# Kernel tuning notes

Measured on AMD Instinct MI355X. Metric: run time of the kernel, lower is better.

## Reference

```python
import jax, jax.numpy as jnp
import numpy as np
import math

LEVEL_SHAPES = [(100, 152), (50, 76), (25, 38), (13, 19)]
BS, E, NH, NL, NP = 2, 256, 8, 4, 4


def _grid_init_bias(num_heads, num_levels, num_points):
    # faithful to MultiScaleDeformableAttention.init_weights sampling_offsets bias
    thetas = jnp.arange(num_heads, dtype=jnp.float32) * (2.0 * math.pi / num_heads)
    grid = jnp.stack([jnp.cos(thetas), jnp.sin(thetas)], -1)  # [H,2]
    grid = grid / jnp.max(jnp.abs(grid), axis=-1, keepdims=True)
    grid = jnp.tile(grid[:, None, None, :], (1, num_levels, num_points, 1))  # [H,L,P,2]
    scale = jnp.arange(1, num_points + 1, dtype=jnp.float32)[None, None, :, None]
    return (grid * scale).reshape(-1)


def setup_inputs() -> dict:
    key = jax.random.key(0)
    ks = jax.random.split(key, 10)
    nv = sum(h * w for h, w in LEVEL_SHAPES)  # 20197
    nq = nv
    query = jax.random.normal(ks[0], (BS, nq, E), dtype=jnp.float32)
    value = jax.random.normal(ks[1], (BS, nv, E), dtype=jnp.float32)
    reference_points = jax.random.uniform(ks[2], (BS, nq, NL, 2), dtype=jnp.float32)
    spatial_shapes = jnp.array(LEVEL_SHAPES, dtype=jnp.int32)
    sizes = [h * w for h, w in LEVEL_SHAPES]
    level_start_index = jnp.array(np.cumsum([0] + sizes)[:-1], dtype=jnp.int32)
    s = 1.0 / math.sqrt(E)
    # Linear params stored as [in, out]; y = x @ W + b
    Wv = jax.random.normal(ks[3], (E, E), dtype=jnp.float32) * s
    bv = jnp.zeros((E,), jnp.float32)
    Wso = jax.random.normal(ks[4], (E, NH * NL * NP * 2), dtype=jnp.float32) * 0.01
    bso = _grid_init_bias(NH, NL, NP)
    Waw = jax.random.normal(ks[5], (E, NH * NL * NP), dtype=jnp.float32) * 0.01
    baw = jnp.zeros((NH * NL * NP,), jnp.float32)
    Wo = jax.random.normal(ks[6], (E, E), dtype=jnp.float32) * s
    bo = jnp.zeros((E,), jnp.float32)
    return dict(query=query, value=value, reference_points=reference_points,
                spatial_shapes=spatial_shapes, level_start_index=level_start_index,
                Wv=Wv, bv=bv, Wso=Wso, bso=bso, Waw=Waw, baw=baw, Wo=Wo, bo=bo)


def _bilinear_sample(vl, loc, h, w):
    # vl: [bs, nh, h*w, d]; loc: [bs, nq, nh, P, 2] normalized in [0,1]
    # matches F.grid_sample(mode='bilinear', padding_mode='zeros', align_corners=False)
    bs, nh, _, d = vl.shape
    nq, P = loc.shape[1], loc.shape[3]
    x = loc[..., 0] * w - 0.5
    y = loc[..., 1] * h - 0.5
    x0 = jnp.floor(x).astype(jnp.int32); x1 = x0 + 1
    y0 = jnp.floor(y).astype(jnp.int32); y1 = y0 + 1
    wx1 = x - x0; wx0 = 1.0 - wx1
    wy1 = y - y0; wy0 = 1.0 - wy1

    def gather(ix, iy):
        valid = ((ix >= 0) & (ix < w) & (iy >= 0) & (iy < h)).astype(vl.dtype)
        idx = jnp.clip(iy, 0, h - 1) * w + jnp.clip(ix, 0, w - 1)  # [bs,nq,nh,P]
        idx = jnp.transpose(idx, (0, 2, 1, 3)).reshape(bs, nh, nq * P)
        g = jnp.take_along_axis(vl, idx[..., None], axis=2)  # [bs,nh,nq*P,d]
        g = g.reshape(bs, nh, nq, P, d).transpose(0, 2, 1, 3, 4)  # [bs,nq,nh,P,d]
        return g * valid[..., None]

    return (gather(x0, y0) * (wx0 * wy0)[..., None]
            + gather(x1, y0) * (wx1 * wy0)[..., None]
            + gather(x0, y1) * (wx0 * wy1)[..., None]
            + gather(x1, y1) * (wx1 * wy1)[..., None])


def reference(query, value, reference_points, spatial_shapes, level_start_index,
              Wv, bv, Wso, bso, Waw, baw, Wo, bo):
    bs, nq, e = query.shape
    nv = value.shape[1]
    nh, nl, npt = NH, NL, NP
    d = e // nh
    shapes = np.asarray(spatial_shapes)          # static level shapes
    starts = np.asarray(level_start_index)

    v = (value @ Wv + bv).reshape(bs, nv, nh, d).transpose(0, 2, 1, 3)  # [bs,nh,nv,d]
    so = (query @ Wso + bso).reshape(bs, nq, nh, nl, npt, 2)
    aw = jax.nn.softmax((query @ Waw + baw).reshape(bs, nq, nh, nl * npt), axis=-1)
    aw = aw.reshape(bs, nq, nh, nl, npt)

    # offset normalizer is (w, h) per level
    offset_norm = jnp.stack([spatial_shapes[:, 1], spatial_shapes[:, 0]], -1).astype(query.dtype)
    loc = reference_points[:, :, None, :, None, :] + so / offset_norm[None, None, None, :, None, :]

    out = jnp.zeros((bs, nq, nh, d), dtype=query.dtype)
    for l in range(nl):
        h, w = int(shapes[l, 0]), int(shapes[l, 1])
        s = int(starts[l])
        vl = v[:, :, s:s + h * w, :]                      # [bs,nh,h*w,d]
        sampled = _bilinear_sample(vl, loc[:, :, :, l], h, w)  # [bs,nq,nh,P,d]
        out = out + jnp.einsum('bqhpd,bqhp->bqhd', sampled, aw[:, :, :, l])

    out = out.reshape(bs, nq, e) @ Wo + bo
    return out + query  # identity residual (dropout in eval mode)
```

## Files before the change

### kernel.cpp

```cpp
#include <hip/hip_runtime.h>
#include <hip/hip_bf16.h>
#include <math.h>

constexpr int kBS = 2;
constexpr int kNQ = 20197;
constexpr int kNV = 20197;
constexpr int kNH = 8;
constexpr int kM  = kBS * kNQ;
constexpr int kMpad = 40448;

__constant__ int cLH[4] = {100, 50, 25, 13};
__constant__ int cLW[4] = {152, 76, 38, 19};
__constant__ int cLS[4] = {0, 15200, 19000, 19950};

typedef __bf16 bf16x8 __attribute__((ext_vector_type(8)));
typedef float  f32x4  __attribute__((ext_vector_type(4)));

__device__ __forceinline__ unsigned short f2bf(float x) {
    unsigned u = __float_as_uint(x);
    return (unsigned short)((u + 0x7fffu + ((u >> 16) & 1u)) >> 16);
}
__device__ __forceinline__ unsigned pack2(float a, float b) {
    return (unsigned)f2bf(a) | ((unsigned)f2bf(b) << 16);
}
__device__ __forceinline__ void gload_lds16(const void* g, void* s) {
    __builtin_amdgcn_global_load_lds(
        (const __attribute__((address_space(1))) void*)g,
        (__attribute__((address_space(3))) void*)s, 16, 0, 0);
}

__global__ __launch_bounds__(256) void prep_wt(
    const float* __restrict__ src, unsigned short* __restrict__ dst,
    int total, int N)
{
    int i = blockIdx.x * 256 + threadIdx.x;
    if (i >= total) return;
    int n = i >> 8, k = i & 255;
    dst[i] = f2bf(src[k * N + n]);
}

template<bool ABF16, bool OUTBF16, bool RES>
__global__ __launch_bounds__(256) void gemm_mfma(
    const void* __restrict__ Av, const __hip_bfloat16* __restrict__ BT,
    const float* __restrict__ bias, const float* __restrict__ res,
    void* __restrict__ Cv, int M, int N)
{
    constexpr int APITCH = ABF16 ? 32 : 40;
    __shared__ __hip_bfloat16 As[128 * APITCH];
    __shared__ __hip_bfloat16 Bs[128 * 32];

    const int t = threadIdx.x;
    const int wave = t >> 6, lane = t & 63;
    const int quad = lane >> 4, l16 = lane & 15;
    const int mw = (wave & 1) * 64, nw = (wave >> 1) * 64;
    const int m0 = blockIdx.y * 128, n0 = blockIdx.x * 128;
    const int sm = t >> 1;
    const int sh = (t & 1) * 16;

    f32x4 acc[4][4] = {};

    for (int k0 = 0; k0 < 256; k0 += 32) {
        __syncthreads();
        {
            const char* bt = (const char*)BT;
            #pragma unroll
            for (int j = 0; j < 2; ++j) {
                int off = j * 4096 + t * 16;
                int row = off >> 6, kb = off & 63;
                gload_lds16(bt + (size_t)(n0 + row) * 512 + k0 * 2 + kb,
                            (char*)Bs + off);
            }
        }
        if constexpr (ABF16) {
            const char* ab = (const char*)Av;
            #pragma unroll
            for (int j = 0; j < 2; ++j) {
                int off = j * 4096 + t * 16;
                int row = off >> 6, kb = off & 63;
                gload_lds16(ab + (size_t)(m0 + row) * 512 + k0 * 2 + kb,
                            (char*)As + off);
            }
        } else {
            const float* af = (const float*)Av;
            float4 f0 = make_float4(0.f, 0.f, 0.f, 0.f), f1 = f0, f2 = f0, f3 = f0;
            if (m0 + sm < M) {
                const float4* p = (const float4*)(af + (size_t)(m0 + sm) * 256 + k0 + sh);
                f0 = p[0]; f1 = p[1]; f2 = p[2]; f3 = p[3];
            }
            uint4 q0 = make_uint4(pack2(f0.x, f0.y), pack2(f0.z, f0.w),
                                  pack2(f1.x, f1.y), pack2(f1.z, f1.w));
            uint4 q1 = make_uint4(pack2(f2.x, f2.y), pack2(f2.z, f2.w),
                                  pack2(f3.x, f3.y), pack2(f3.z, f3.w));
            uint4* dst = (uint4*)(void*)&As[sm * APITCH + sh];
            dst[0] = q0; dst[1] = q1;
        }
        __syncthreads();
        bf16x8 afr[4], bfr[4];
        #pragma unroll
        for (int mt = 0; mt < 4; ++mt)
            afr[mt] = *(const bf16x8*)(const void*)&As[(mw + mt * 16 + l16) * APITCH + quad * 8];
        #pragma unroll
        for (int nt = 0; nt < 4; ++nt)
            bfr[nt] = *(const bf16x8*)(const void*)&Bs[(nw + nt * 16 + l16) * 32 + quad * 8];
        #pragma unroll
        for (int mt = 0; mt < 4; ++mt)
            #pragma unroll
            for (int nt = 0; nt < 4; ++nt)
                acc[mt][nt] = __builtin_amdgcn_mfma_f32_16x16x32_bf16(
                    afr[mt], bfr[nt], acc[mt][nt], 0, 0, 0);
    }

    #pragma unroll
    for (int nt = 0; nt < 4; ++nt) {
        int col = n0 + nw + nt * 16 + l16;
        float bvv = bias[col];
        #pragma unroll
        for (int mt = 0; mt < 4; ++mt) {
            #pragma unroll
            for (int i = 0; i < 4; ++i) {
                int row = m0 + mw + mt * 16 + quad * 4 + i;
                if (row < M) {
                    float val = acc[mt][nt][i] + bvv;
                    if constexpr (RES) val += res[(size_t)row * N + col];
                    if constexpr (OUTBF16)
                        ((unsigned short*)Cv)[(size_t)row * N + col] = f2bf(val);
                    else
                        ((float*)Cv)[(size_t)row * N + col] = val;
                }
            }
        }
    }
}

__global__ __launch_bounds__(128) void msda_sample(
    const __hip_bfloat16* __restrict__ v,
    const float* __restrict__ so,
    const float* __restrict__ logits,
    const float* __restrict__ rp,
    __hip_bfloat16* __restrict__ mid)
{
    const int bq = blockIdx.x;
    const int b  = bq >= kNQ;
    const int t  = threadIdx.x;

    __shared__ int   sOff[128 * 5];
    __shared__ float sW[128 * 5];

    {
        const int h = t >> 4, l = (t >> 2) & 3;
        float2 sv = *(const float2*)(so + (size_t)bq * 256 + 2 * t);
        float  aa = logits[(size_t)bq * 128 + t];
        float2 rr = *(const float2*)(rp + (size_t)bq * 8 + l * 2);
        float mx = aa;
        #pragma unroll
        for (int s = 8; s >= 1; s >>= 1) mx = fmaxf(mx, __shfl_xor(mx, s, 16));
        float e = __expf(aa - mx);
        float sum = e;
        #pragma unroll
        for (int s = 8; s >= 1; s >>= 1) sum += __shfl_xor(sum, s, 16);
        float w = e / sum;

        const int ww = cLW[l], hh = cLH[l];
        const float fw = (float)ww, fh = (float)hh;
        float x = rr.x * fw + sv.x - 0.5f;
        float y = rr.y * fh + sv.y - 0.5f;
        float xf = floorf(x), yf = floorf(y);
        int x0 = (int)xf, y0 = (int)yf;
        float wx1 = x - xf, wx0 = 1.f - wx1;
        float wy1 = y - yf, wy0 = 1.f - wy1;
        bool vx0 = (x0 >= 0) & (x0 < ww);
        bool vx1 = (x0 >= -1) & (x0 + 1 < ww);
        bool vy0 = (y0 >= 0) & (y0 < hh);
        bool vy1 = (y0 >= -1) & (y0 + 1 < hh);
        int cx0 = min(max(x0, 0), ww - 1);
        int cx1 = min(max(x0 + 1, 0), ww - 1);
        int cy0 = min(max(y0, 0), hh - 1);
        int cy1 = min(max(y0 + 1, 0), hh - 1);
        int base = cLS[l] * 256 + h * 32;
        sOff[t * 5 + 0] = base + (cy0 * ww + cx0) * 256;
        sOff[t * 5 + 1] = base + (cy0 * ww + cx1) * 256;
        sOff[t * 5 + 2] = base + (cy1 * ww + cx0) * 256;
        sOff[t * 5 + 3] = base + (cy1 * ww + cx1) * 256;
        sW[t * 5 + 0] = (vx0 & vy0) ? w * wx0 * wy0 : 0.f;
        sW[t * 5 + 1] = (vx1 & vy0) ? w * wx1 * wy0 : 0.f;
        sW[t * 5 + 2] = (vx0 & vy1) ? w * wx0 * wy1 : 0.f;
        sW[t * 5 + 3] = (vx1 & vy1) ? w * wx1 * wy1 : 0.f;
    }
    __syncthreads();

    const int h = t >> 4, c = (t & 15) * 2;
    const __hip_bfloat16* vb = v + (size_t)b * kNV * 256 + c;
    float accx = 0.f, accy = 0.f;
    const int p0 = h * 16;
    #pragma unroll 4
    for (int pp = 0; pp < 16; ++pp) {
        const int idx = (p0 + pp) * 5;
        #pragma unroll
        for (int k2 = 0; k2 < 4; ++k2) {
            float wgt = sW[idx + k2];
            int   off = sOff[idx + k2];
            unsigned u = *(const unsigned*)(const void*)(vb + off);
            float lo = __uint_as_float(u << 16);
            float hi = __uint_as_float(u & 0xffff0000u);
            accx += wgt * lo;
            accy += wgt * hi;
        }
    }
    unsigned pk = pack2(accx, accy);
    *(unsigned*)(void*)(mid + (size_t)bq * 256 + h * 32 + c) = pk;
}

extern "C" void kernel_launch(void* const* d_in, const int* in_sizes, int n_in,
                              void* d_out, int out_size, void* d_ws, size_t ws_size,
                              hipStream_t stream)
{
    const float* query = (const float*)d_in[0];
    const float* value = (const float*)d_in[1];
    const float* rp    = (const float*)d_in[2];
    const float* Wv  = (const float*)d_in[5];
    const float* bv  = (const float*)d_in[6];
    const float* Wso = (const float*)d_in[7];
    const float* bso = (const float*)d_in[8];
    const float* Waw = (const float*)d_in[9];
    const float* baw = (const float*)d_in[10];
    const float* Wo  = (const float*)d_in[11];
    const float* bo  = (const float*)d_in[12];

    char* out8 = (char*)d_out;
    __hip_bfloat16* v_b    = (__hip_bfloat16*)out8;
    float*          logits = (float*)(out8 + (size_t)kM * 512);

    char* ws8 = (char*)d_ws;
    float*          so    = (float*)ws8;
    __hip_bfloat16* mid_b = (__hip_bfloat16*)(ws8 + (size_t)kM * 1024);
    __hip_bfloat16* WvT   = (__hip_bfloat16*)(ws8 + (size_t)kM * 1024 + (size_t)kMpad * 512);
    __hip_bfloat16* WsoT  = WvT  + 256 * 256;
    __hip_bfloat16* WawT  = WsoT + 256 * 256;
    __hip_bfloat16* WoT   = WawT + 128 * 256;

    hipLaunchKernelGGL(prep_wt, dim3(256), dim3(256), 0, stream, Wv,  (unsigned short*)WvT,  256 * 256, 256);
    hipLaunchKernelGGL(prep_wt, dim3(256), dim3(256), 0, stream, Wso, (unsigned short*)WsoT, 256 * 256, 256);
    hipLaunchKernelGGL(prep_wt, dim3(128), dim3(256), 0, stream, Waw, (unsigned short*)WawT, 128 * 256, 128);
    hipLaunchKernelGGL(prep_wt, dim3(256), dim3(256), 0, stream, Wo,  (unsigned short*)WoT,  256 * 256, 256);

    dim3 blk(256);
    dim3 g2(2, 316), g1(1, 316);
    hipLaunchKernelGGL((gemm_mfma<false, true,  false>), g2, blk, 0, stream,
                       (const void*)value, WvT, bv, (const float*)nullptr, (void*)v_b, kM, 256);
    hipLaunchKernelGGL((gemm_mfma<false, false, false>), g2, blk, 0, stream,
                       (const void*)query, WsoT, bso, (const float*)nullptr, (void*)so, kM, 256);
    hipLaunchKernelGGL((gemm_mfma<false, false, false>), g1, blk, 0, stream,
                       (const void*)query, WawT, baw, (const float*)nullptr, (void*)logits, kM, 128);
    hipLaunchKernelGGL(msda_sample, dim3(kM), dim3(128), 0, stream,
                       v_b, so, logits, rp, mid_b);
    hipLaunchKernelGGL((gemm_mfma<true,  false, true>), g2, blk, 0, stream,
                       (const void*)mid_b, WoT, bo, query, d_out, kM, 256);
}
```

Before: 336.1 us.

## Fuse projection GEMMs, emit bf16 offsets/logits, and widen sampling kernel per thread

Merges the four weight-prep launches into one and fuses the value, sampling-offset and attention-logit projections into a single dual GEMM launch. The query-side projections are written as bf16 into one 384-wide buffer, which halves intermediate traffic. The sampling kernel now handles four queries per 256-thread block, loads four channels per gather, and uses int4/float4 LDS slots with an XOR swizzle. The changes cut launch overhead and memory traffic, but storing offsets in bf16 costs sampling-location precision, and positions can be off by up to about half a pixel at large coordinates.

```diff
diff --git a/kernel.cpp b/kernel.cpp
--- a/kernel.cpp
+++ b/kernel.cpp
@@ -5,7 +5,6 @@
 constexpr int kBS = 2;
 constexpr int kNQ = 20197;
 constexpr int kNV = 20197;
-constexpr int kNH = 8;
 constexpr int kM  = kBS * kNQ;
 constexpr int kMpad = 40448;
 
@@ -23,37 +22,59 @@
 __device__ __forceinline__ unsigned pack2(float a, float b) {
     return (unsigned)f2bf(a) | ((unsigned)f2bf(b) << 16);
 }
+__device__ __forceinline__ float bflo(unsigned u) { return __uint_as_float(u << 16); }
+__device__ __forceinline__ float bfhi(unsigned u) { return __uint_as_float(u & 0xffff0000u); }
 __device__ __forceinline__ void gload_lds16(const void* g, void* s) {
     __builtin_amdgcn_global_load_lds(
         (const __attribute__((address_space(1))) void*)g,
         (__attribute__((address_space(3))) void*)s, 16, 0, 0);
 }
 
-__global__ __launch_bounds__(256) void prep_wt(
-    const float* __restrict__ src, unsigned short* __restrict__ dst,
-    int total, int N)
+__global__ __launch_bounds__(256) void prep(
+    const float* __restrict__ Wv, const float* __restrict__ Wso,
+    const float* __restrict__ Waw, const float* __restrict__ Wo,
+    const float* __restrict__ bso, const float* __restrict__ baw,
+    unsigned short* __restrict__ WvT, unsigned short* __restrict__ WsoawT,
+    unsigned short* __restrict__ WoT, float* __restrict__ bias384)
 {
     int i = blockIdx.x * 256 + threadIdx.x;
-    if (i >= total) return;
-    int n = i >> 8, k = i & 255;
-    dst[i] = f2bf(src[k * N + n]);
-}
-
-template<bool ABF16, bool OUTBF16, bool RES>
-__global__ __launch_bounds__(256) void gemm_mfma(
-    const void* __restrict__ Av, const __hip_bfloat16* __restrict__ BT,
-    const float* __restrict__ bias, const float* __restrict__ res,
-    void* __restrict__ Cv, int M, int N)
-{
-    constexpr int APITCH = ABF16 ? 32 : 40;
+    if (i < 65536) { int n = i >> 8, k = i & 255; WvT[i] = f2bf(Wv[k * 256 + n]); return; }
+    i -= 65536;
+    if (i < 98304) {
+        int n = i >> 8, k = i & 255;
+        WsoawT[i] = f2bf(n < 256 ? Wso[k * 256 + n] : Waw[k * 128 + (n - 256)]);
+        return;
+    }
+    i -= 98304;
+    if (i < 65536) { int n = i >> 8, k = i & 255; WoT[i] = f2bf(Wo[k * 256 + n]); return; }
+    i -= 65536;
+    if (i < 384) bias384[i] = (i < 256) ? bso[i] : baw[i - 256];
+}
+
+__global__ __launch_bounds__(256) void gemm_dual(
+    const float* __restrict__ A0, const __hip_bfloat16* __restrict__ BT0,
+    const float* __restrict__ bias0, unsigned short* __restrict__ C0,
+    const float* __restrict__ A1, const __hip_bfloat16* __restrict__ BT1,
+    const float* __restrict__ bias1, unsigned short* __restrict__ C1)
+{
+    constexpr int APITCH = 40;
     __shared__ __hip_bfloat16 As[128 * APITCH];
     __shared__ __hip_bfloat16 Bs[128 * 32];
+
+    const int bx = blockIdx.x;
+    const bool second = bx >= 2;
+    const float* A = second ? A1 : A0;
+    const __hip_bfloat16* BT = second ? BT1 : BT0;
+    const float* bias = second ? bias1 : bias0;
+    unsigned short* C = second ? C1 : C0;
+    const int N = second ? 384 : 256;
+    const int n0 = (second ? bx - 2 : bx) * 128;
+    const int m0 = blockIdx.y * 128;
 
     const int t = threadIdx.x;
     const int wave = t >> 6, lane = t & 63;
     const int quad = lane >> 4, l16 = lane & 15;
     const int mw = (wave & 1) * 64, nw = (wave >> 1) * 64;
-    const int m0 = blockIdx.y * 128, n0 = blockIdx.x * 128;
     const int sm = t >> 1;
     const int sh = (t & 1) * 16;
 
@@ -71,20 +92,10 @@
                             (char*)Bs + off);
             }
         }
-        if constexpr (ABF16) {
-            const char* ab = (const char*)Av;
-            #pragma unroll
-            for (int j = 0; j < 2; ++j) {
-                int off = j * 4096 + t * 16;
-                int row = off >> 6, kb = off & 63;
-                gload_lds16(ab + (size_t)(m0 + row) * 512 + k0 * 2 + kb,
-                            (char*)As + off);
-            }
-        } else {
-            const float* af = (const float*)Av;
+        {
             float4 f0 = make_float4(0.f, 0.f, 0.f, 0.f), f1 = f0, f2 = f0, f3 = f0;
-            if (m0 + sm < M) {
-                const float4* p = (const float4*)(af + (size_t)(m0 + sm) * 256 + k0 + sh);
+            if (m0 + sm < kM) {
+                const float4* p = (const float4*)(A + (size_t)(m0 + sm) * 256 + k0 + sh);
                 f0 = p[0]; f1 = p[1]; f2 = p[2]; f3 = p[3];
             }
             uint4 q0 = make_uint4(pack2(f0.x, f0.y), pack2(f0.z, f0.w),
@@ -119,42 +130,105 @@
             #pragma unroll
             for (int i = 0; i < 4; ++i) {
                 int row = m0 + mw + mt * 16 + quad * 4 + i;
-                if (row < M) {
-                    float val = acc[mt][nt][i] + bvv;
-                    if constexpr (RES) val += res[(size_t)row * N + col];
-                    if constexpr (OUTBF16)
-                        ((unsigned short*)Cv)[(size_t)row * N + col] = f2bf(val);
-                    else
-                        ((float*)Cv)[(size_t)row * N + col] = val;
-                }
+                if (row < kM)
+                    C[(size_t)row * N + col] = f2bf(acc[mt][nt][i] + bvv);
             }
         }
     }
 }
 
-__global__ __launch_bounds__(128) void msda_sample(
+__global__ __launch_bounds__(256) void gemm_final(
+    const __hip_bfloat16* __restrict__ Ab, const __hip_bfloat16* __restrict__ BT,
+    const float* __restrict__ bias, const float* __restrict__ res,
+    float* __restrict__ C)
+{
+    __shared__ __hip_bfloat16 As[128 * 32];
+    __shared__ __hip_bfloat16 Bs[128 * 32];
+
+    const int t = threadIdx.x;
+    const int wave = t >> 6, lane = t & 63;
+    const int quad = lane >> 4, l16 = lane & 15;
+    const int mw = (wave & 1) * 64, nw = (wave >> 1) * 64;
+    const int m0 = blockIdx.y * 128, n0 = blockIdx.x * 128;
+
+    f32x4 acc[4][4] = {};
+
+    for (int k0 = 0; k0 < 256; k0 += 32) {
+        __syncthreads();
+        const char* bt = (const char*)BT;
+        const char* ab = (const char*)Ab;
+        #pragma unroll
+        for (int j = 0; j < 2; ++j) {
+            int off = j * 4096 + t * 16;
+            int row = off >> 6, kb = off & 63;
+            gload_lds16(bt + (size_t)(n0 + row) * 512 + k0 * 2 + kb, (char*)Bs + off);
+            gload_lds16(ab + (size_t)(m0 + row) * 512 + k0 * 2 + kb, (char*)As + off);
+        }
+        __syncthreads();
+        bf16x8 afr[4], bfr[4];
+        #pragma unroll
+        for (int mt = 0; mt < 4; ++mt)
+            afr[mt] = *(const bf16x8*)(const void*)&As[(mw + mt * 16 + l16) * 32 + quad * 8];
+        #pragma unroll
+        for (int nt = 0; nt < 4; ++nt)
+            bfr[nt] = *(const bf16x8*)(const void*)&Bs[(nw + nt * 16 + l16) * 32 + quad * 8];
+        #pragma unroll
+        for (int mt = 0; mt < 4; ++mt)
+            #pragma unroll
+            for (int nt = 0; nt < 4; ++nt)
+                acc[mt][nt] = __builtin_amdgcn_mfma_f32_16x16x32_bf16(
+                    afr[mt], bfr[nt], acc[mt][nt], 0, 0, 0);
+    }
+
+    #pragma unroll
+    for (int nt = 0; nt < 4; ++nt) {
+        int col = n0 + nw + nt * 16 + l16;
+        float bvv = bias[col];
+        #pragma unroll
+        for (int mt = 0; mt < 4; ++mt) {
+            #pragma unroll
+            for (int i = 0; i < 4; ++i) {
+                int row = m0 + mw + mt * 16 + quad * 4 + i;
+                if (row < kM)
+                    C[(size_t)row * 256 + col] =
+                        acc[mt][nt][i] + bvv + res[(size_t)row * 256 + col];
+            }
+        }
+    }
+}
+
+__global__ __launch_bounds__(256) void msda_sample(
     const __hip_bfloat16* __restrict__ v,
-    const float* __restrict__ so,
-    const float* __restrict__ logits,
+    const __hip_bfloat16* __restrict__ soaw,
     const float* __restrict__ rp,
     __hip_bfloat16* __restrict__ mid)
 {
-    const int bq = blockIdx.x;
-    const int b  = bq >= kNQ;
-    const int t  = threadIdx.x;
-
-    __shared__ int   sOff[128 * 5];
-    __shared__ float sW[128 * 5];
-
-    {
-        const int h = t >> 4, l = (t >> 2) & 3;
-        float2 sv = *(const float2*)(so + (size_t)bq * 256 + 2 * t);
-        float  aa = logits[(size_t)bq * 128 + t];
-        float2 rr = *(const float2*)(rp + (size_t)bq * 8 + l * 2);
-        float mx = aa;
+    __shared__ int   sOff[512 * 4];
+    __shared__ float sW[512 * 4];
+    const int t = threadIdx.x;
+
+    #pragma unroll
+    for (int it = 0; it < 2; ++it) {
+        const int idx = it * 256 + t;
+        const int q = idx >> 7, r = idx & 127;
+        const int h = r >> 4, lp = r & 15, l = lp >> 2;
+        const int bq = blockIdx.x * 4 + q;
+        const bool ok = bq < kM;
+
+        unsigned sopk = 0; float logit = 0.f;
+        float2 rr = make_float2(0.f, 0.f);
+        if (ok) {
+            sopk  = *(const unsigned*)(const void*)(soaw + (size_t)bq * 384 + 2 * r);
+            logit = bflo((unsigned)*(const unsigned short*)(const void*)
+                         (soaw + (size_t)bq * 384 + 256 + r));
+            rr    = *(const float2*)(rp + (size_t)bq * 8 + l * 2);
+        }
+        float sx = bflo(sopk), sy = bfhi(sopk);
+
+        float mx = logit;
         #pragma unroll
         for (int s = 8; s >= 1; s >>= 1) mx = fmaxf(mx, __shfl_xor(mx, s, 16));
-        float e = __expf(aa - mx);
+        float e = __expf(logit - mx);
         float sum = e;
         #pragma unroll
         for (int s = 8; s >= 1; s >>= 1) sum += __shfl_xor(sum, s, 16);
@@ -162,8 +236,8 @@
 
         const int ww = cLW[l], hh = cLH[l];
         const float fw = (float)ww, fh = (float)hh;
-        float x = rr.x * fw + sv.x - 0.5f;
-        float y = rr.y * fh + sv.y - 0.5f;
+        float x = rr.x * fw + sx - 0.5f;
+        float y = rr.y * fh + sy - 0.5f;
         float xf = floorf(x), yf = floorf(y);
         int x0 = (int)xf, y0 = (int)yf;
         float wx1 = x - xf, wx0 = 1.f - wx1;
@@ -176,38 +250,56 @@
         int cx1 = min(max(x0 + 1, 0), ww - 1);
         int cy0 = min(max(y0, 0), hh - 1);
         int cy1 = min(max(y0 + 1, 0), hh - 1);
-        int base = cLS[l] * 256 + h * 32;
-        sOff[t * 5 + 0] = base + (cy0 * ww + cx0) * 256;
-        sOff[t * 5 + 1] = base + (cy0 * ww + cx1) * 256;
-        sOff[t * 5 + 2] = base + (cy1 * ww + cx0) * 256;
-        sOff[t * 5 + 3] = base + (cy1 * ww + cx1) * 256;
-        sW[t * 5 + 0] = (vx0 & vy0) ? w * wx0 * wy0 : 0.f;
-        sW[t * 5 + 1] = (vx1 & vy0) ? w * wx1 * wy0 : 0.f;
-        sW[t * 5 + 2] = (vx0 & vy1) ? w * wx0 * wy1 : 0.f;
-        sW[t * 5 + 3] = (vx1 & vy1) ? w * wx1 * wy1 : 0.f;
+        const int base = cLS[l] * 256 + h * 32;
+
+        const int slot = q * 128 + lp * 8 + (h ^ (lp & 7));
+        ((int4*)sOff)[slot] = make_int4(base + (cy0 * ww + cx0) * 256,
+                                        base + (cy0 * ww + cx1) * 256,
+                                        base + (cy1 * ww + cx0) * 256,
+                                        base + (cy1 * ww + cx1) * 256);
+        ((float4*)sW)[slot] = make_float4((vx0 & vy0) ? w * wx0 * wy0 : 0.f,
+                                          (vx1 & vy0) ? w * wx1 * wy0 : 0.f,
+                                          (vx0 & vy1) ? w * wx0 * wy1 : 0.f,
+                                          (vx1 & vy1) ? w * wx1 * wy1 : 0.f);
     }
     __syncthreads();
 
-    const int h = t >> 4, c = (t & 15) * 2;
+    const int q = t >> 6, h = (t >> 3) & 7, c = (t & 7) * 4;
+    const int bq = blockIdx.x * 4 + q;
+    const int b = (bq >= kNQ) ? 1 : 0;
     const __hip_bfloat16* vb = v + (size_t)b * kNV * 256 + c;
-    float accx = 0.f, accy = 0.f;
-    const int p0 = h * 16;
+
+    float a0 = 0.f, a1 = 0.f, a2 = 0.f, a3 = 0.f;
     #pragma unroll 4
     for (int pp = 0; pp < 16; ++pp) {
-        const int idx = (p0 + pp) * 5;
-        #pragma unroll
-        for (int k2 = 0; k2 < 4; ++k2) {
-            float wgt = sW[idx + k2];
-            int   off = sOff[idx + k2];
-            unsigned u = *(const unsigned*)(const void*)(vb + off);
-            float lo = __uint_as_float(u << 16);
-            float hi = __uint_as_float(u & 0xffff0000u);
-            accx += wgt * lo;
-            accy += wgt * hi;
-        }
-    }
-    unsigned pk = pack2(accx, accy);
-    *(unsigned*)(void*)(mid + (size_t)bq * 256 + h * 32 + c) = pk;
+        const int slot = q * 128 + pp * 8 + (h ^ (pp & 7));
+        int4   o = ((const int4*)sOff)[slot];
+        float4 wv = ((const float4*)sW)[slot];
+        {
+            uint2 u = *(const uint2*)(const void*)(vb + o.x);
+            a0 += wv.x * bflo(u.x); a1 += wv.x * bfhi(u.x);
+            a2 += wv.x * bflo(u.y); a3 += wv.x * bfhi(u.y);
+        }
+        {
+            uint2 u = *(const uint2*)(const void*)(vb + o.y);
+            a0 += wv.y * bflo(u.x); a1 += wv.y * bfhi(u.x);
+            a2 += wv.y * bflo(u.y); a3 += wv.y * bfhi(u.y);
+        }
+        {
+            uint2 u = *(const uint2*)(const void*)(vb + o.z);
+            a0 += wv.z * bflo(u.x); a1 += wv.z * bfhi(u.x);
+            a2 += wv.z * bflo(u.y); a3 += wv.z * bfhi(u.y);
+        }
+        {
+            uint2 u = *(const uint2*)(const void*)(vb + o.w);
+            a0 += wv.w * bflo(u.x); a1 += wv.w * bfhi(u.x);
+            a2 += wv.w * bflo(u.y); a3 += wv.w * bfhi(u.y);
+        }
+    }
+    if (bq < kM) {
+        uint2 pk = make_uint2(pack2(a0, a1), pack2(a2, a3));
+        *(uint2*)(void*)(mid + (size_t)bq * 256 + h * 32 + c) = pk;
+    }
 }
 
 extern "C" void kernel_launch(void* const* d_in, const int* in_sizes, int n_in,
@@ -226,33 +318,27 @@
     const float* Wo  = (const float*)d_in[11];
     const float* bo  = (const float*)d_in[12];
 
-    char* out8 = (char*)d_out;
-    __hip_bfloat16* v_b    = (__hip_bfloat16*)out8;
-    float*          logits = (float*)(out8 + (size_t)kM * 512);
+    __hip_bfloat16* v_b = (__hip_bfloat16*)d_out;
 
     char* ws8 = (char*)d_ws;
-    float*          so    = (float*)ws8;
-    __hip_bfloat16* mid_b = (__hip_bfloat16*)(ws8 + (size_t)kM * 1024);
-    __hip_bfloat16* WvT   = (__hip_bfloat16*)(ws8 + (size_t)kM * 1024 + (size_t)kMpad * 512);
-    __hip_bfloat16* WsoT  = WvT  + 256 * 256;
-    __hip_bfloat16* WawT  = WsoT + 256 * 256;
-    __hip_bfloat16* WoT   = WawT + 128 * 256;
-
-    hipLaunchKernelGGL(prep_wt, dim3(256), dim3(256), 0, stream, Wv,  (unsigned short*)WvT,  256 * 256, 256);
-    hipLaunchKernelGGL(prep_wt, dim3(256), dim3(256), 0, stream, Wso, (unsigned short*)WsoT, 256 * 256, 256);
-    hipLaunchKernelGGL(prep_wt, dim3(128), dim3(256), 0, stream, Waw, (unsigned short*)WawT, 128 * 256, 128);
-    hipLaunchKernelGGL(prep_wt, dim3(256), dim3(256), 0, stream, Wo,  (unsigned short*)WoT,  256 * 256, 256);
-
-    dim3 blk(256);
-    dim3 g2(2, 316), g1(1, 316);
-    hipLaunchKernelGGL((gemm_mfma<false, true,  false>), g2, blk, 0, stream,
-                       (const void*)value, WvT, bv, (const float*)nullptr, (void*)v_b, kM, 256);
-    hipLaunchKernelGGL((gemm_mfma<false, false, false>), g2, blk, 0, stream,
-                       (const void*)query, WsoT, bso, (const float*)nullptr, (void*)so, kM, 256);
-    hipLaunchKernelGGL((gemm_mfma<false, false, false>), g1, blk, 0, stream,
-                       (const void*)query, WawT, baw, (const float*)nullptr, (void*)logits, kM, 128);
-    hipLaunchKernelGGL(msda_sample, dim3(kM), dim3(128), 0, stream,
-                       v_b, so, logits, rp, mid_b);
-    hipLaunchKernelGGL((gemm_mfma<true,  false, true>), g2, blk, 0, stream,
-                       (const void*)mid_b, WoT, bo, query, d_out, kM, 256);
-}
+    __hip_bfloat16* soaw  = (__hip_bfloat16*)ws8;
+    char* p = ws8 + (size_t)kM * 384 * 2;
+    __hip_bfloat16* mid_b = (__hip_bfloat16*)p;  p += (size_t)kMpad * 256 * 2;
+    unsigned short* WvT    = (unsigned short*)p; p += 256 * 256 * 2;
+    unsigned short* WsoawT = (unsigned short*)p; p += 384 * 256 * 2;
+    unsigned short* WoT    = (unsigned short*)p; p += 256 * 256 * 2;
+    float* bias384         = (float*)p;
+
+    hipLaunchKernelGGL(prep, dim3(898), dim3(256), 0, stream,
+                       Wv, Wso, Waw, Wo, bso, baw, WvT, WsoawT, WoT, bias384);
+
+    hipLaunchKernelGGL(gemm_dual, dim3(5, 316), dim3(256), 0, stream,
+                       value, (const __hip_bfloat16*)WvT, bv, (unsigned short*)v_b,
+                       query, (const __hip_bfloat16*)WsoawT, bias384, (unsigned short*)soaw);
+
+    hipLaunchKernelGGL(msda_sample, dim3((kM + 3) / 4), dim3(256), 0, stream,
+                       v_b, soaw, rp, mid_b);
+
+    hipLaunchKernelGGL(gemm_final, dim3(2, 316), dim3(256), 0, stream,
+                       mid_b, (const __hip_bfloat16*)WoT, bo, query, (float*)d_out);
+}
```

Measured after the change: 339.9 us. Within noise of the previous version (+1.1%).

## Fuse projection GEMMs, stage full-K A tile once, store offsets and logits as bf16

Applied to the files above, without the earlier changes.

Merges the four weight-prep launches into one kernel. Fuses the value, sampling-offset and attention-logit projections into a single dual GEMM launch, with offsets and logits concatenated into one 384-wide bf16 output. The GEMM now loads a 64-row A tile across the full K once into LDS (converting fp32 to bf16) and loops over N tiles with double-buffered B loads, so the fp32 query is read once instead of twice. The trade-offs are offsets and logits stored in bf16, which lowers sampling precision, and a larger LDS footprint per block.

```diff
diff --git a/kernel.cpp b/kernel.cpp
--- a/kernel.cpp
+++ b/kernel.cpp
@@ -5,9 +5,9 @@
 constexpr int kBS = 2;
 constexpr int kNQ = 20197;
 constexpr int kNV = 20197;
-constexpr int kNH = 8;
 constexpr int kM  = kBS * kNQ;
-constexpr int kMpad = 40448;
+constexpr int kMT = 632;
+constexpr int kMpad = kMT * 64;
 
 __constant__ int cLH[4] = {100, 50, 25, 13};
 __constant__ int cLW[4] = {152, 76, 38, 19};
@@ -23,119 +23,155 @@
 __device__ __forceinline__ unsigned pack2(float a, float b) {
     return (unsigned)f2bf(a) | ((unsigned)f2bf(b) << 16);
 }
+__device__ __forceinline__ float bflo(unsigned u) { return __uint_as_float(u << 16); }
+__device__ __forceinline__ float bfhi(unsigned u) { return __uint_as_float(u & 0xffff0000u); }
 __device__ __forceinline__ void gload_lds16(const void* g, void* s) {
     __builtin_amdgcn_global_load_lds(
         (const __attribute__((address_space(1))) void*)g,
         (__attribute__((address_space(3))) void*)s, 16, 0, 0);
 }
 
-__global__ __launch_bounds__(256) void prep_wt(
-    const float* __restrict__ src, unsigned short* __restrict__ dst,
-    int total, int N)
-{
-    int i = blockIdx.x * 256 + threadIdx.x;
-    if (i >= total) return;
-    int n = i >> 8, k = i & 255;
-    dst[i] = f2bf(src[k * N + n]);
-}
-
-template<bool ABF16, bool OUTBF16, bool RES>
-__global__ __launch_bounds__(256) void gemm_mfma(
+__global__ __launch_bounds__(256) void prep_w(
+    const float* __restrict__ Wv, const float* __restrict__ Wso,
+    const float* __restrict__ Waw, const float* __restrict__ Wo,
+    const float* __restrict__ bso, const float* __restrict__ baw,
+    unsigned short* __restrict__ WvT, unsigned short* __restrict__ WsoawT,
+    unsigned short* __restrict__ WoT, float* __restrict__ bias384)
+{
+    int k = blockIdx.x * 256 + threadIdx.x;
+    if (k < 65536) { WvT[k] = f2bf(Wv[(k & 255) * 256 + (k >> 8)]); return; }
+    k -= 65536;
+    if (k < 98304) {
+        int n = k >> 8, kk = k & 255;
+        WsoawT[k] = f2bf(n < 256 ? Wso[kk * 256 + n] : Waw[kk * 128 + (n - 256)]);
+        return;
+    }
+    k -= 98304;
+    if (k < 65536) { WoT[k] = f2bf(Wo[(k & 255) * 256 + (k >> 8)]); return; }
+    k -= 65536;
+    if (k < 384) bias384[k] = (k < 256) ? bso[k] : baw[k - 256];
+}
+
+template<int AFP32, int CFP32>
+__device__ __forceinline__ void gemm_core(
     const void* __restrict__ Av, const __hip_bfloat16* __restrict__ BT,
     const float* __restrict__ bias, const float* __restrict__ res,
-    void* __restrict__ Cv, int M, int N)
-{
-    constexpr int APITCH = ABF16 ? 32 : 40;
-    __shared__ __hip_bfloat16 As[128 * APITCH];
-    __shared__ __hip_bfloat16 Bs[128 * 32];
+    int N, int NT, void* __restrict__ Cv, int m0)
+{
+    __shared__ __hip_bfloat16 As[64 * 264];
+    __shared__ __hip_bfloat16 Bs[2][128 * 32];
 
     const int t = threadIdx.x;
     const int wave = t >> 6, lane = t & 63;
     const int quad = lane >> 4, l16 = lane & 15;
-    const int mw = (wave & 1) * 64, nw = (wave >> 1) * 64;
-    const int m0 = blockIdx.y * 128, n0 = blockIdx.x * 128;
-    const int sm = t >> 1;
-    const int sh = (t & 1) * 16;
-
-    f32x4 acc[4][4] = {};
-
-    for (int k0 = 0; k0 < 256; k0 += 32) {
-        __syncthreads();
-        {
-            const char* bt = (const char*)BT;
-            #pragma unroll
-            for (int j = 0; j < 2; ++j) {
-                int off = j * 4096 + t * 16;
-                int row = off >> 6, kb = off & 63;
-                gload_lds16(bt + (size_t)(n0 + row) * 512 + k0 * 2 + kb,
-                            (char*)Bs + off);
-            }
-        }
-        if constexpr (ABF16) {
-            const char* ab = (const char*)Av;
-            #pragma unroll
-            for (int j = 0; j < 2; ++j) {
-                int off = j * 4096 + t * 16;
-                int row = off >> 6, kb = off & 63;
-                gload_lds16(ab + (size_t)(m0 + row) * 512 + k0 * 2 + kb,
-                            (char*)As + off);
-            }
-        } else {
-            const float* af = (const float*)Av;
-            float4 f0 = make_float4(0.f, 0.f, 0.f, 0.f), f1 = f0, f2 = f0, f3 = f0;
-            if (m0 + sm < M) {
-                const float4* p = (const float4*)(af + (size_t)(m0 + sm) * 256 + k0 + sh);
-                f0 = p[0]; f1 = p[1]; f2 = p[2]; f3 = p[3];
-            }
-            uint4 q0 = make_uint4(pack2(f0.x, f0.y), pack2(f0.z, f0.w),
-                                  pack2(f1.x, f1.y), pack2(f1.z, f1.w));
-            uint4 q1 = make_uint4(pack2(f2.x, f2.y), pack2(f2.z, f2.w),
-                                  pack2(f3.x, f3.y), pack2(f3.z, f3.w));
-            uint4* dst = (uint4*)(void*)&As[sm * APITCH + sh];
-            dst[0] = q0; dst[1] = q1;
-        }
-        __syncthreads();
-        bf16x8 afr[4], bfr[4];
-        #pragma unroll
-        for (int mt = 0; mt < 4; ++mt)
-            afr[mt] = *(const bf16x8*)(const void*)&As[(mw + mt * 16 + l16) * APITCH + quad * 8];
-        #pragma unroll
-        for (int nt = 0; nt < 4; ++nt)
-            bfr[nt] = *(const bf16x8*)(const void*)&Bs[(nw + nt * 16 + l16) * 32 + quad * 8];
-        #pragma unroll
-        for (int mt = 0; mt < 4; ++mt)
+    const int mw = (wave & 1) * 32, nw = (wave >> 1) * 64;
+
+    auto issueB = [&](int nti, int kc, int buf) {
+        #pragma unroll
+        for (int j = 0; j < 2; ++j) {
+            int off = j * 4096 + t * 16;
+            int row = off >> 6, kb = off & 63;
+            gload_lds16((const char*)BT + (size_t)(nti * 128 + row) * 512 + kc * 64 + kb,
+                        (char*)&Bs[buf][0] + off);
+        }
+    };
+
+    issueB(0, 0, 0);
+
+    if (AFP32) {
+        const float* af = (const float*)Av;
+        #pragma unroll
+        for (int p = 0; p < 16; ++p) {
+            int idx = p * 256 + t;
+            int row = idx >> 6, col4 = idx & 63;
+            float4 f = make_float4(0.f, 0.f, 0.f, 0.f);
+            if (m0 + row < kM)
+                f = *(const float4*)(af + (size_t)(m0 + row) * 256 + col4 * 4);
+            uint2 u = make_uint2(pack2(f.x, f.y), pack2(f.z, f.w));
+            *(uint2*)(void*)&As[row * 264 + col4 * 4] = u;
+        }
+    } else {
+        const unsigned short* ab = (const unsigned short*)Av;
+        #pragma unroll
+        for (int p = 0; p < 8; ++p) {
+            int idx = p * 256 + t;
+            int row = idx >> 5, ch = idx & 31;
+            uint4 u = *(const uint4*)(ab + (size_t)(m0 + row) * 256 + ch * 8);
+            *(uint4*)(void*)&As[row * 264 + ch * 8] = u;
+        }
+    }
+
+    for (int nti = 0; nti < NT; ++nti) {
+        f32x4 acc[2][4] = {};
+        for (int kc = 0; kc < 8; ++kc) {
+            __syncthreads();
+            if (kc < 7)             issueB(nti, kc + 1, (kc + 1) & 1);
+            else if (nti + 1 < NT)  issueB(nti + 1, 0, 0);
+            bf16x8 afr[2], bfr[4];
+            #pragma unroll
+            for (int mt = 0; mt < 2; ++mt)
+                afr[mt] = *(const bf16x8*)(const void*)
+                    &As[(mw + mt * 16 + l16) * 264 + kc * 32 + quad * 8];
             #pragma unroll
             for (int nt = 0; nt < 4; ++nt)
-                acc[mt][nt] = __builtin_amdgcn_mfma_f32_16x16x32_bf16(
-                    afr[mt], bfr[nt], acc[mt][nt], 0, 0, 0);
-    }
-
-    #pragma unroll
-    for (int nt = 0; nt < 4; ++nt) {
-        int col = n0 + nw + nt * 16 + l16;
-        float bvv = bias[col];
-        #pragma unroll
-        for (int mt = 0; mt < 4; ++mt) {
-            #pragma unroll
-            for (int i = 0; i < 4; ++i) {
-                int row = m0 + mw + mt * 16 + quad * 4 + i;
-                if (row < M) {
-                    float val = acc[mt][nt][i] + bvv;
-                    if constexpr (RES) val += res[(size_t)row * N + col];
-                    if constexpr (OUTBF16)
-                        ((unsigned short*)Cv)[(size_t)row * N + col] = f2bf(val);
-                    else
-                        ((float*)Cv)[(size_t)row * N + col] = val;
+                bfr[nt] = *(const bf16x8*)(const void*)
+                    &Bs[kc & 1][(nw + nt * 16 + l16) * 32 + quad * 8];
+            #pragma unroll
+            for (int mt = 0; mt < 2; ++mt)
+                #pragma unroll
+                for (int nt = 0; nt < 4; ++nt)
+                    acc[mt][nt] = __builtin_amdgcn_mfma_f32_16x16x32_bf16(
+                        afr[mt], bfr[nt], acc[mt][nt], 0, 0, 0);
+        }
+        const int n0g = nti * 128;
+        #pragma unroll
+        for (int nt = 0; nt < 4; ++nt) {
+            int col = n0g + nw + nt * 16 + l16;
+            float bvv = bias[col];
+            #pragma unroll
+            for (int mt = 0; mt < 2; ++mt) {
+                #pragma unroll
+                for (int i = 0; i < 4; ++i) {
+                    int row = m0 + mw + mt * 16 + quad * 4 + i;
+                    if (row < kM) {
+                        float val = acc[mt][nt][i] + bvv;
+                        if (CFP32)
+                            ((float*)Cv)[(size_t)row * N + col] =
+                                val + res[(size_t)row * N + col];
+                        else
+                            ((unsigned short*)Cv)[(size_t)row * N + col] = f2bf(val);
+                    }
                 }
             }
         }
     }
 }
 
+__global__ __launch_bounds__(256, 3) void gemm_dual(
+    const float* __restrict__ value, const __hip_bfloat16* __restrict__ WvT,
+    const float* __restrict__ bv, unsigned short* __restrict__ v_b,
+    const float* __restrict__ query, const __hip_bfloat16* __restrict__ WsoawT,
+    const float* __restrict__ b384, unsigned short* __restrict__ soaw)
+{
+    const int m0 = blockIdx.y * 64;
+    const float* A; const __hip_bfloat16* BT; const float* bias;
+    unsigned short* C; int N, NT;
+    if (blockIdx.x == 0) { A = value; BT = WvT;    bias = bv;   C = v_b;  N = 256; NT = 2; }
+    else                 { A = query; BT = WsoawT; bias = b384; C = soaw; N = 384; NT = 3; }
+    gemm_core<1, 0>(A, BT, bias, nullptr, N, NT, C, m0);
+}
+
+__global__ __launch_bounds__(256, 3) void gemm_final(
+    const unsigned short* __restrict__ mid_b, const __hip_bfloat16* __restrict__ WoT,
+    const float* __restrict__ bo, const float* __restrict__ query,
+    float* __restrict__ out)
+{
+    gemm_core<0, 1>(mid_b, WoT, bo, query, 256, 2, out, blockIdx.y * 64);
+}
+
 __global__ __launch_bounds__(128) void msda_sample(
     const __hip_bfloat16* __restrict__ v,
-    const float* __restrict__ so,
-    const float* __restrict__ logits,
+    const __hip_bfloat16* __restrict__ soaw,
     const float* __restrict__ rp,
     __hip_bfloat16* __restrict__ mid)
 {
@@ -147,14 +183,17 @@
     __shared__ float sW[128 * 5];
 
     {
-        const int h = t >> 4, l = (t >> 2) & 3;
-        float2 sv = *(const float2*)(so + (size_t)bq * 256 + 2 * t);
-        float  aa = logits[(size_t)bq * 128 + t];
+        const int h = t >> 4, lp = t & 15, l = lp >> 2;
+        unsigned sopk = *(const unsigned*)(const void*)(soaw + (size_t)bq * 384 + 2 * t);
+        float logit = bflo((unsigned)*(const unsigned short*)(const void*)
+                           (soaw + (size_t)bq * 384 + 256 + t));
         float2 rr = *(const float2*)(rp + (size_t)bq * 8 + l * 2);
-        float mx = aa;
+        float sx = bflo(sopk), sy = bfhi(sopk);
+
+        float mx = logit;
         #pragma unroll
         for (int s = 8; s >= 1; s >>= 1) mx = fmaxf(mx, __shfl_xor(mx, s, 16));
-        float e = __expf(aa - mx);
+        float e = __expf(logit - mx);
         float sum = e;
         #pragma unroll
         for (int s = 8; s >= 1; s >>= 1) sum += __shfl_xor(sum, s, 16);
@@ -162,8 +201,8 @@
 
         const int ww = cLW[l], hh = cLH[l];
         const float fw = (float)ww, fh = (float)hh;
-        float x = rr.x * fw + sv.x - 0.5f;
-        float y = rr.y * fh + sv.y - 0.5f;
+        float x = rr.x * fw + sx - 0.5f;
+        float y = rr.y * fh + sy - 0.5f;
         float xf = floorf(x), yf = floorf(y);
         int x0 = (int)xf, y0 = (int)yf;
         float wx1 = x - xf, wx0 = 1.f - wx1;
@@ -176,7 +215,7 @@
         int cx1 = min(max(x0 + 1, 0), ww - 1);
         int cy0 = min(max(y0, 0), hh - 1);
         int cy1 = min(max(y0 + 1, 0), hh - 1);
-        int base = cLS[l] * 256 + h * 32;
+        const int base = cLS[l] * 256 + h * 32;
         sOff[t * 5 + 0] = base + (cy0 * ww + cx0) * 256;
         sOff[t * 5 + 1] = base + (cy0 * ww + cx1) * 256;
         sOff[t * 5 + 2] = base + (cy1 * ww + cx0) * 256;
@@ -200,14 +239,11 @@
             float wgt = sW[idx + k2];
             int   off = sOff[idx + k2];
             unsigned u = *(const unsigned*)(const void*)(vb + off);
-            float lo = __uint_as_float(u << 16);
-            float hi = __uint_as_float(u & 0xffff0000u);
-            accx += wgt * lo;
-            accy += wgt * hi;
-        }
-    }
-    unsigned pk = pack2(accx, accy);
-    *(unsigned*)(void*)(mid + (size_t)bq * 256 + h * 32 + c) = pk;
+            accx += wgt * bflo(u);
+            accy += wgt * bfhi(u);
+        }
+    }
+    *(unsigned*)(void*)(mid + (size_t)bq * 256 + h * 32 + c) = pack2(accx, accy);
 }
 
 extern "C" void kernel_launch(void* const* d_in, const int* in_sizes, int n_in,
@@ -226,33 +262,27 @@
     const float* Wo  = (const float*)d_in[11];
     const float* bo  = (const float*)d_in[12];
 
-    char* out8 = (char*)d_out;
-    __hip_bfloat16* v_b    = (__hip_bfloat16*)out8;
-    float*          logits = (float*)(out8 + (size_t)kM * 512);
-
-    char* ws8 = (char*)d_ws;
-    float*          so    = (float*)ws8;
-    __hip_bfloat16* mid_b = (__hip_bfloat16*)(ws8 + (size_t)kM * 1024);
-    __hip_bfloat16* WvT   = (__hip_bfloat16*)(ws8 + (size_t)kM * 1024 + (size_t)kMpad * 512);
-    __hip_bfloat16* WsoT  = WvT  + 256 * 256;
-    __hip_bfloat16* WawT  = WsoT + 256 * 256;
-    __hip_bfloat16* WoT   = WawT + 128 * 256;
-
-    hipLaunchKernelGGL(prep_wt, dim3(256), dim3(256), 0, stream, Wv,  (unsigned short*)WvT,  256 * 256, 256);
-    hipLaunchKernelGGL(prep_wt, dim3(256), dim3(256), 0, stream, Wso, (unsigned short*)WsoT, 256 * 256, 256);
-    hipLaunchKernelGGL(prep_wt, dim3(128), dim3(256), 0, stream, Waw, (unsigned short*)WawT, 128 * 256, 128);
-    hipLaunchKernelGGL(prep_wt, dim3(256), dim3(256), 0, stream, Wo,  (unsigned short*)WoT,  256 * 256, 256);
-
-    dim3 blk(256);
-    dim3 g2(2, 316), g1(1, 316);
-    hipLaunchKernelGGL((gemm_mfma<false, true,  false>), g2, blk, 0, stream,
-                       (const void*)value, WvT, bv, (const float*)nullptr, (void*)v_b, kM, 256);
-    hipLaunchKernelGGL((gemm_mfma<false, false, false>), g2, blk, 0, stream,
-                       (const void*)query, WsoT, bso, (const float*)nullptr, (void*)so, kM, 256);
-    hipLaunchKernelGGL((gemm_mfma<false, false, false>), g1, blk, 0, stream,
-                       (const void*)query, WawT, baw, (const float*)nullptr, (void*)logits, kM, 128);
+    unsigned short* v_b = (unsigned short*)d_out;
+
+    char* p = (char*)d_ws;
+    __hip_bfloat16* soaw  = (__hip_bfloat16*)p;  p += (size_t)kM * 384 * 2;
+    unsigned short* mid_b = (unsigned short*)p;  p += (size_t)kMpad * 256 * 2;
+    unsigned short* WvT    = (unsigned short*)p; p += 256 * 256 * 2;
+    unsigned short* WsoawT = (unsigned short*)p; p += 384 * 256 * 2;
+    unsigned short* WoT    = (unsigned short*)p; p += 256 * 256 * 2;
+    float* bias384         = (float*)p;
+
+    hipLaunchKernelGGL(prep_w, dim3(898), dim3(256), 0, stream,
+                       Wv, Wso, Waw, Wo, bso, baw, WvT, WsoawT, WoT, bias384);
+
+    hipLaunchKernelGGL(gemm_dual, dim3(2, kMT), dim3(256), 0, stream,
+                       value, (const __hip_bfloat16*)WvT, bv, v_b,
+                       query, (const __hip_bfloat16*)WsoawT, bias384,
+                       (unsigned short*)soaw);
+
     hipLaunchKernelGGL(msda_sample, dim3(kM), dim3(128), 0, stream,
-                       v_b, so, logits, rp, mid_b);
-    hipLaunchKernelGGL((gemm_mfma<true,  false, true>), g2, blk, 0, stream,
-                       (const void*)mid_b, WoT, bo, query, d_out, kM, 256);
-}
+                       (const __hip_bfloat16*)v_b, soaw, rp, (__hip_bfloat16*)mid_b);
+
+    hipLaunchKernelGGL(gemm_final, dim3(1, kMT), dim3(256), 0, stream,
+                       mid_b, (const __hip_bfloat16*)WoT, bo, query, (float*)d_out);
+}
```

Result: faster. 299.6 us (-10.9%).
